# Kernel optimization log

Hardware: AMD Instinct MI355X
Metric: run time of the kernel (lower is better)

The kernel has to match this reference:

```python
import jax, jax.numpy as jnp
import numpy as np

BETA = 0.25  # commitment loss weight (args.beta)
K = 1024     # num_codebook_vectors
D = 256      # latent_dim


def setup_inputs() -> dict:
    key = jax.random.key(0)
    k1, k2 = jax.random.split(key)
    z = jax.random.normal(k1, (64, 32, 32, D), dtype=jnp.float32)
    # matches tf.random_uniform_initializer(-1/K, 1/K) on shape (latent_dim, K)
    embedding = jax.random.uniform(k2, (D, K), dtype=jnp.float32,
                                   minval=-1.0 / K, maxval=1.0 / K)
    return {"z": z, "embedding": embedding}


def reference(z, embedding):
    # z: [B,H,W,D]; embedding: [D,K]
    z_flat = z.reshape(-1, D)  # [N,D]
    # pairwise squared distances: ||z||^2 + ||e||^2 - 2 z.e  -> [N,K]
    d = (jnp.sum(z_flat * z_flat, axis=1, keepdims=True)
         + jnp.sum(embedding * embedding, axis=0)
         - 2.0 * (z_flat @ embedding))
    min_encoding_indices = jnp.argmin(d, axis=1)  # [N] int
    # one-hot @ embedding.T is exactly a row gather of embedding.T
    z_q = jnp.take(embedding.T, min_encoding_indices, axis=0).reshape(z.shape)
    commitment_loss = BETA * jnp.mean((jax.lax.stop_gradient(z_q) - z) ** 2)
    codebook_loss = jnp.mean((z_q - jax.lax.stop_gradient(z)) ** 2)
    loss = commitment_loss + codebook_loss
    z_q_st = z + jax.lax.stop_gradient(z_q - z)  # straight-through estimator
    return (z_q_st, min_encoding_indices, loss)
```

## Files before the change

### kernel.cpp

```cpp
#include <hip/hip_runtime.h>
#include <math.h>

#define KCODES 1024
#define DDIM   256
#define NROWS  65536
#define BM     64
#define NT     512

__device__ __forceinline__ int swz(int d, int r) {
    return (d << 6) + ((((r) >> 2) ^ ((d >> 2) & 15)) << 2) + (r & 3);
}

__global__ __launch_bounds__(256) void enorm_kernel(const float* __restrict__ e,
                                                    float* __restrict__ enorm,
                                                    float* __restrict__ loss_acc) {
    const int k = blockIdx.x * 256 + threadIdx.x;
    if (k == 0) *loss_acc = 0.f;
    float s = 0.f;
    for (int d = 0; d < DDIM; ++d) {
        const float v = e[(size_t)d * KCODES + k];
        s = __fadd_rn(s, __fmul_rn(v, v));
    }
    enorm[k] = s;
}

__global__ __launch_bounds__(256) void etrans_kernel(const float* __restrict__ e,
                                                     float* __restrict__ eT) {
    const int d = blockIdx.x;
    const int t = threadIdx.x;
    const float4 v = *reinterpret_cast<const float4*>(e + (size_t)d * KCODES + t * 4);
    eT[(size_t)(t * 4 + 0) * DDIM + d] = v.x;
    eT[(size_t)(t * 4 + 1) * DDIM + d] = v.y;
    eT[(size_t)(t * 4 + 2) * DDIM + d] = v.z;
    eT[(size_t)(t * 4 + 3) * DDIM + d] = v.w;
}

__global__ __launch_bounds__(NT, 4) void vq_main(const float* __restrict__ z,
                                                 const float* __restrict__ e,
                                                 const float* __restrict__ enorm,
                                                 const float* __restrict__ eT,
                                                 float* __restrict__ out_zq,
                                                 float* __restrict__ out_idx,
                                                 float* __restrict__ loss_acc) {
    __shared__ __align__(16) float A[DDIM * BM];
    __shared__ float zn_s[BM];
    __shared__ int   kmin_s[BM];
    __shared__ float wsum_s[8];

    const int tid  = threadIdx.x;
    const int lane = tid & 63;
    const int wv   = tid >> 6;
    const int row0 = blockIdx.x * BM;

    for (int p = 0; p < 8; ++p) {
        const int row = p * 8 + wv;
        const int d0  = lane * 4;
        const float4 v = *reinterpret_cast<const float4*>(z + (size_t)(row0 + row) * DDIM + d0);
        A[swz(d0 + 0, row)] = v.x;
        A[swz(d0 + 1, row)] = v.y;
        A[swz(d0 + 2, row)] = v.z;
        A[swz(d0 + 3, row)] = v.w;
    }
    __syncthreads();

    if (tid < BM) {
        const int r = tid;
        float hsum[2];
        #pragma unroll
        for (int h = 0; h < 2; ++h) {
            const int base = h * 128;
            float rp[8];
            #pragma unroll
            for (int j = 0; j < 8; ++j) {
                const float v = A[swz(base + j, r)];
                rp[j] = __fmul_rn(v, v);
            }
            for (int i = 8; i < 128; i += 8) {
                #pragma unroll
                for (int j = 0; j < 8; ++j) {
                    const float v = A[swz(base + i + j, r)];
                    rp[j] = __fadd_rn(rp[j], __fmul_rn(v, v));
                }
            }
            hsum[h] = __fadd_rn(__fadd_rn(__fadd_rn(rp[0], rp[1]), __fadd_rn(rp[2], rp[3])),
                                __fadd_rn(__fadd_rn(rp[4], rp[5]), __fadd_rn(rp[6], rp[7])));
        }
        zn_s[r] = __fadd_rn(hsum[0], hsum[1]);
    }
    __syncthreads();

    const int rg = tid >> 5;
    const int cg = tid & 31;

    float rmin[4] = {INFINITY, INFINITY, INFINITY, INFINITY};
    int   ridx[4] = {0, 0, 0, 0};

    for (int ct = 0; ct < 8; ++ct) {
        const int c0 = (ct << 7) + (cg << 2);
        const float4 en4 = *reinterpret_cast<const float4*>(enorm + c0);
        const float* __restrict__ bp = e + c0;

        float acc[4][4];
        #pragma unroll
        for (int jj = 0; jj < 4; ++jj)
            #pragma unroll
            for (int i = 0; i < 4; ++i) acc[jj][i] = 0.f;

        for (int db = 0; db < DDIM; db += 16) {
            float4 bb[16];
            #pragma unroll
            for (int j = 0; j < 16; ++j)
                bb[j] = *reinterpret_cast<const float4*>(bp + (size_t)((db + j) << 10));
            #pragma unroll
            for (int s = 0; s < 4; ++s) {
                const int t = ((db >> 2) + s) & 15;
                const float* ap = &A[((db + (s << 2)) << 6) + ((rg ^ t) << 2)];
                #pragma unroll
                for (int j = 0; j < 4; ++j) {
                    const float4 a = *reinterpret_cast<const float4*>(ap + (j << 6));
                    const float4 b = bb[(s << 2) | j];
                    acc[0][0] = fmaf(a.x, b.x, acc[0][0]);
                    acc[0][1] = fmaf(a.x, b.y, acc[0][1]);
                    acc[0][2] = fmaf(a.x, b.z, acc[0][2]);
                    acc[0][3] = fmaf(a.x, b.w, acc[0][3]);
                    acc[1][0] = fmaf(a.y, b.x, acc[1][0]);
                    acc[1][1] = fmaf(a.y, b.y, acc[1][1]);
                    acc[1][2] = fmaf(a.y, b.z, acc[1][2]);
                    acc[1][3] = fmaf(a.y, b.w, acc[1][3]);
                    acc[2][0] = fmaf(a.z, b.x, acc[2][0]);
                    acc[2][1] = fmaf(a.z, b.y, acc[2][1]);
                    acc[2][2] = fmaf(a.z, b.z, acc[2][2]);
                    acc[2][3] = fmaf(a.z, b.w, acc[2][3]);
                    acc[3][0] = fmaf(a.w, b.x, acc[3][0]);
                    acc[3][1] = fmaf(a.w, b.y, acc[3][1]);
                    acc[3][2] = fmaf(a.w, b.z, acc[3][2]);
                    acc[3][3] = fmaf(a.w, b.w, acc[3][3]);
                }
            }
        }

        const float en[4] = {en4.x, en4.y, en4.z, en4.w};
        #pragma unroll
        for (int jj = 0; jj < 4; ++jj) {
            const float zn = zn_s[(rg << 2) + jj];
            #pragma unroll
            for (int i = 0; i < 4; ++i) {
                const float t = __fadd_rn(zn, en[i]);
                const float s = __fmaf_rn(-2.f, acc[jj][i], t);
                if (s < rmin[jj]) { rmin[jj] = s; ridx[jj] = c0 + i; }
            }
        }
    }

    #pragma unroll
    for (int jj = 0; jj < 4; ++jj) {
        float bv = rmin[jj];
        int   bi = ridx[jj];
        #pragma unroll
        for (int mask = 16; mask >= 1; mask >>= 1) {
            const float ov = __shfl_xor(bv, mask);
            const int   oi = __shfl_xor(bi, mask);
            if (ov < bv || (ov == bv && oi < bi)) { bv = ov; bi = oi; }
        }
        if (cg == 0) {
            const int row = (rg << 2) + jj;
            kmin_s[row] = bi;
            out_idx[row0 + row] = (float)bi;
        }
    }
    __syncthreads();

    float part = 0.f;
    for (int p = 0; p < 8; ++p) {
        const int row = p * 8 + wv;
        const int d0  = lane * 4;
        const int kk  = kmin_s[row];
        const float4 q = *reinterpret_cast<const float4*>(eT + (size_t)kk * DDIM + d0);
        const float z0 = A[swz(d0 + 0, row)];
        const float z1 = A[swz(d0 + 1, row)];
        const float z2 = A[swz(d0 + 2, row)];
        const float z3 = A[swz(d0 + 3, row)];
        float dx;
        dx = q.x - z0; part = fmaf(dx, dx, part);
        dx = q.y - z1; part = fmaf(dx, dx, part);
        dx = q.z - z2; part = fmaf(dx, dx, part);
        dx = q.w - z3; part = fmaf(dx, dx, part);
        *reinterpret_cast<float4*>(out_zq + (size_t)(row0 + row) * DDIM + d0) = q;
    }
    #pragma unroll
    for (int off = 32; off > 0; off >>= 1) part += __shfl_down(part, off);
    if (lane == 0) wsum_s[wv] = part;
    __syncthreads();
    if (tid == 0) {
        float s = 0.f;
        #pragma unroll
        for (int i = 0; i < 8; ++i) s += wsum_s[i];
        atomicAdd(loss_acc, s);
    }
}

__global__ void finalize_kernel(const float* __restrict__ loss_acc,
                                float* __restrict__ out_loss) {
    const float m = __fdiv_rn(*loss_acc, 16777216.f);
    out_loss[0] = __fadd_rn(__fmul_rn(0.25f, m), m);
}

extern "C" void kernel_launch(void* const* d_in, const int* in_sizes, int n_in,
                              void* d_out, int out_size, void* d_ws, size_t ws_size,
                              hipStream_t stream) {
    const float* z = (const float*)d_in[0];
    const float* e = (const float*)d_in[1];

    float* out_zq   = (float*)d_out;
    float* out_idx  = out_zq + (size_t)NROWS * DDIM;
    float* out_loss = out_idx + NROWS;

    float* loss_acc = (float*)d_ws;
    float* enorm    = (float*)((char*)d_ws + 256);
    float* eT       = (float*)((char*)d_ws + 8192);

    enorm_kernel<<<KCODES / 256, 256, 0, stream>>>(e, enorm, loss_acc);
    etrans_kernel<<<DDIM, 256, 0, stream>>>(e, eT);
    vq_main<<<NROWS / BM, NT, 0, stream>>>(z, e, enorm, eT, out_zq, out_idx, loss_acc);
    finalize_kernel<<<1, 1, 0, stream>>>(loss_acc, out_loss);
}
```

Measured before the change: 703.3 us.

## Retile distance GEMM to 8x4 per thread, tile transpose, nontemporal I/O

The main kernel's register tile changes from 4 rows x 4 codes to 8 rows x 4 codes per thread. Each wave now owns 8 rows and sweeps 256 codes per pass, so each codebook load from global/L2 feeds twice as many FMAs, and the argmin reduction spans the full wave. The codebook transpose now goes through a padded shared-memory tile for coalesced writes. Loads of z and stores of z_q use nontemporal hints. The larger accumulator array raises register pressure, which may reduce occupancy under the 4-block launch bound.

New measurement: 590.1 us. 16.1% less time.

```diff
diff --git a/kernel.cpp b/kernel.cpp
--- a/kernel.cpp
+++ b/kernel.cpp
@@ -6,6 +6,8 @@
 #define NROWS  65536
 #define BM     64
 #define NT     512
+
+typedef float f4 __attribute__((ext_vector_type(4)));
 
 __device__ __forceinline__ int swz(int d, int r) {
     return (d << 6) + ((((r) >> 2) ^ ((d >> 2) & 15)) << 2) + (r & 3);
@@ -26,13 +28,31 @@
 
 __global__ __launch_bounds__(256) void etrans_kernel(const float* __restrict__ e,
                                                      float* __restrict__ eT) {
-    const int d = blockIdx.x;
-    const int t = threadIdx.x;
-    const float4 v = *reinterpret_cast<const float4*>(e + (size_t)d * KCODES + t * 4);
-    eT[(size_t)(t * 4 + 0) * DDIM + d] = v.x;
-    eT[(size_t)(t * 4 + 1) * DDIM + d] = v.y;
-    eT[(size_t)(t * 4 + 2) * DDIM + d] = v.z;
-    eT[(size_t)(t * 4 + 3) * DDIM + d] = v.w;
+    __shared__ float tile[64][65];
+    const int k0 = blockIdx.x << 6;
+    const int d0 = blockIdx.y << 6;
+    const int tr = threadIdx.x >> 4;
+    const int tc = threadIdx.x & 15;
+    #pragma unroll
+    for (int p = 0; p < 4; ++p) {
+        const int d = (p << 4) + tr;
+        const f4 v = *reinterpret_cast<const f4*>(e + (size_t)(d0 + d) * KCODES + k0 + (tc << 2));
+        tile[(tc << 2) + 0][d] = v[0];
+        tile[(tc << 2) + 1][d] = v[1];
+        tile[(tc << 2) + 2][d] = v[2];
+        tile[(tc << 2) + 3][d] = v[3];
+    }
+    __syncthreads();
+    #pragma unroll
+    for (int p = 0; p < 4; ++p) {
+        const int k = (p << 4) + tr;
+        f4 w;
+        w[0] = tile[k][(tc << 2) + 0];
+        w[1] = tile[k][(tc << 2) + 1];
+        w[2] = tile[k][(tc << 2) + 2];
+        w[3] = tile[k][(tc << 2) + 3];
+        *reinterpret_cast<f4*>(eT + (size_t)(k0 + k) * DDIM + d0 + (tc << 2)) = w;
+    }
 }
 
 __global__ __launch_bounds__(NT, 4) void vq_main(const float* __restrict__ z,
@@ -55,11 +75,12 @@
     for (int p = 0; p < 8; ++p) {
         const int row = p * 8 + wv;
         const int d0  = lane * 4;
-        const float4 v = *reinterpret_cast<const float4*>(z + (size_t)(row0 + row) * DDIM + d0);
-        A[swz(d0 + 0, row)] = v.x;
-        A[swz(d0 + 1, row)] = v.y;
-        A[swz(d0 + 2, row)] = v.z;
-        A[swz(d0 + 3, row)] = v.w;
+        const f4 v = __builtin_nontemporal_load(
+            reinterpret_cast<const f4*>(z + (size_t)(row0 + row) * DDIM + d0));
+        A[swz(d0 + 0, row)] = v[0];
+        A[swz(d0 + 1, row)] = v[1];
+        A[swz(d0 + 2, row)] = v[2];
+        A[swz(d0 + 3, row)] = v[3];
     }
     __syncthreads();
 
@@ -89,81 +110,68 @@
     }
     __syncthreads();
 
-    const int rg = tid >> 5;
-    const int cg = tid & 31;
-
-    float rmin[4] = {INFINITY, INFINITY, INFINITY, INFINITY};
-    int   ridx[4] = {0, 0, 0, 0};
-
-    for (int ct = 0; ct < 8; ++ct) {
-        const int c0 = (ct << 7) + (cg << 2);
-        const float4 en4 = *reinterpret_cast<const float4*>(enorm + c0);
+    float rmin[8] = {INFINITY, INFINITY, INFINITY, INFINITY,
+                     INFINITY, INFINITY, INFINITY, INFINITY};
+    int   ridx[8] = {0, 0, 0, 0, 0, 0, 0, 0};
+
+    const int g0 = wv << 1;
+    for (int ct = 0; ct < 4; ++ct) {
+        const int c0 = (ct << 8) + (lane << 2);
+        const f4 en4 = *reinterpret_cast<const f4*>(enorm + c0);
         const float* __restrict__ bp = e + c0;
 
-        float acc[4][4];
-        #pragma unroll
-        for (int jj = 0; jj < 4; ++jj)
-            #pragma unroll
-            for (int i = 0; i < 4; ++i) acc[jj][i] = 0.f;
-
-        for (int db = 0; db < DDIM; db += 16) {
-            float4 bb[16];
-            #pragma unroll
-            for (int j = 0; j < 16; ++j)
-                bb[j] = *reinterpret_cast<const float4*>(bp + (size_t)((db + j) << 10));
-            #pragma unroll
-            for (int s = 0; s < 4; ++s) {
-                const int t = ((db >> 2) + s) & 15;
-                const float* ap = &A[((db + (s << 2)) << 6) + ((rg ^ t) << 2)];
+        float acc[8][4];
+        #pragma unroll
+        for (int r = 0; r < 8; ++r)
+            #pragma unroll
+            for (int i = 0; i < 4; ++i) acc[r][i] = 0.f;
+
+        for (int db = 0; db < DDIM; db += 8) {
+            f4 bb[8];
+            #pragma unroll
+            for (int j = 0; j < 8; ++j)
+                bb[j] = *reinterpret_cast<const f4*>(bp + (size_t)((db + j) << 10));
+            #pragma unroll
+            for (int j = 0; j < 8; ++j) {
+                const int d  = db + j;
+                const int tt = (d >> 2) & 15;
+                const f4 a0 = *reinterpret_cast<const f4*>(&A[(d << 6) + (((g0 | 0) ^ tt) << 2)]);
+                const f4 a1 = *reinterpret_cast<const f4*>(&A[(d << 6) + (((g0 | 1) ^ tt) << 2)]);
+                const f4 b  = bb[j];
                 #pragma unroll
-                for (int j = 0; j < 4; ++j) {
-                    const float4 a = *reinterpret_cast<const float4*>(ap + (j << 6));
-                    const float4 b = bb[(s << 2) | j];
-                    acc[0][0] = fmaf(a.x, b.x, acc[0][0]);
-                    acc[0][1] = fmaf(a.x, b.y, acc[0][1]);
-                    acc[0][2] = fmaf(a.x, b.z, acc[0][2]);
-                    acc[0][3] = fmaf(a.x, b.w, acc[0][3]);
-                    acc[1][0] = fmaf(a.y, b.x, acc[1][0]);
-                    acc[1][1] = fmaf(a.y, b.y, acc[1][1]);
-                    acc[1][2] = fmaf(a.y, b.z, acc[1][2]);
-                    acc[1][3] = fmaf(a.y, b.w, acc[1][3]);
-                    acc[2][0] = fmaf(a.z, b.x, acc[2][0]);
-                    acc[2][1] = fmaf(a.z, b.y, acc[2][1]);
-                    acc[2][2] = fmaf(a.z, b.z, acc[2][2]);
-                    acc[2][3] = fmaf(a.z, b.w, acc[2][3]);
-                    acc[3][0] = fmaf(a.w, b.x, acc[3][0]);
-                    acc[3][1] = fmaf(a.w, b.y, acc[3][1]);
-                    acc[3][2] = fmaf(a.w, b.z, acc[3][2]);
-                    acc[3][3] = fmaf(a.w, b.w, acc[3][3]);
-                }
-            }
-        }
-
-        const float en[4] = {en4.x, en4.y, en4.z, en4.w};
-        #pragma unroll
-        for (int jj = 0; jj < 4; ++jj) {
-            const float zn = zn_s[(rg << 2) + jj];
+                for (int r = 0; r < 4; ++r)
+                    #pragma unroll
+                    for (int i = 0; i < 4; ++i) {
+                        acc[r][i]     = fmaf(a0[r], b[i], acc[r][i]);
+                        acc[4 + r][i] = fmaf(a1[r], b[i], acc[4 + r][i]);
+                    }
+            }
+        }
+
+        #pragma unroll
+        for (int r8 = 0; r8 < 8; ++r8) {
+            const float zn = zn_s[(wv << 3) + r8];
             #pragma unroll
             for (int i = 0; i < 4; ++i) {
-                const float t = __fadd_rn(zn, en[i]);
-                const float s = __fmaf_rn(-2.f, acc[jj][i], t);
-                if (s < rmin[jj]) { rmin[jj] = s; ridx[jj] = c0 + i; }
-            }
-        }
-    }
-
-    #pragma unroll
-    for (int jj = 0; jj < 4; ++jj) {
-        float bv = rmin[jj];
-        int   bi = ridx[jj];
-        #pragma unroll
-        for (int mask = 16; mask >= 1; mask >>= 1) {
+                const float t = __fadd_rn(zn, en4[i]);
+                const float s = __fmaf_rn(-2.f, acc[r8][i], t);
+                if (s < rmin[r8]) { rmin[r8] = s; ridx[r8] = c0 + i; }
+            }
+        }
+    }
+
+    #pragma unroll
+    for (int r8 = 0; r8 < 8; ++r8) {
+        float bv = rmin[r8];
+        int   bi = ridx[r8];
+        #pragma unroll
+        for (int mask = 32; mask >= 1; mask >>= 1) {
             const float ov = __shfl_xor(bv, mask);
             const int   oi = __shfl_xor(bi, mask);
             if (ov < bv || (ov == bv && oi < bi)) { bv = ov; bi = oi; }
         }
-        if (cg == 0) {
-            const int row = (rg << 2) + jj;
+        if (lane == 0) {
+            const int row = (wv << 3) + r8;
             kmin_s[row] = bi;
             out_idx[row0 + row] = (float)bi;
         }
@@ -175,17 +183,17 @@
         const int row = p * 8 + wv;
         const int d0  = lane * 4;
         const int kk  = kmin_s[row];
-        const float4 q = *reinterpret_cast<const float4*>(eT + (size_t)kk * DDIM + d0);
+        const f4 q = *reinterpret_cast<const f4*>(eT + (size_t)kk * DDIM + d0);
         const float z0 = A[swz(d0 + 0, row)];
         const float z1 = A[swz(d0 + 1, row)];
         const float z2 = A[swz(d0 + 2, row)];
         const float z3 = A[swz(d0 + 3, row)];
         float dx;
-        dx = q.x - z0; part = fmaf(dx, dx, part);
-        dx = q.y - z1; part = fmaf(dx, dx, part);
-        dx = q.z - z2; part = fmaf(dx, dx, part);
-        dx = q.w - z3; part = fmaf(dx, dx, part);
-        *reinterpret_cast<float4*>(out_zq + (size_t)(row0 + row) * DDIM + d0) = q;
+        dx = q[0] - z0; part = fmaf(dx, dx, part);
+        dx = q[1] - z1; part = fmaf(dx, dx, part);
+        dx = q[2] - z2; part = fmaf(dx, dx, part);
+        dx = q[3] - z3; part = fmaf(dx, dx, part);
+        __builtin_nontemporal_store(q, reinterpret_cast<f4*>(out_zq + (size_t)(row0 + row) * DDIM + d0));
     }
     #pragma unroll
     for (int off = 32; off > 0; off >>= 1) part += __shfl_down(part, off);
@@ -220,7 +228,7 @@
     float* eT       = (float*)((char*)d_ws + 8192);
 
     enorm_kernel<<<KCODES / 256, 256, 0, stream>>>(e, enorm, loss_acc);
-    etrans_kernel<<<DDIM, 256, 0, stream>>>(e, eT);
+    etrans_kernel<<<dim3(KCODES / 64, DDIM / 64), 256, 0, stream>>>(e, eT);
     vq_main<<<NROWS / BM, NT, 0, stream>>>(z, e, enorm, eT, out_zq, out_idx, loss_acc);
     finalize_kernel<<<1, 1, 0, stream>>>(loss_acc, out_loss);
 }
```
